# Optimization experiments

Measured on AMD Instinct MI355X. Metric: run time of the kernel, lower is better.

The kernel has to match this reference:

```python
import jax, jax.numpy as jnp
import numpy as np

B, T, C, H = 2, 2048, 1024, 16
HD = C // H  # head dim 64


def setup_inputs() -> dict:
    key = jax.random.key(0)
    k1, k2, k3, k4, k5 = jax.random.split(key, 5)
    s = 0.02
    return {
        "x": jax.random.normal(k1, (B, T, C), dtype=jnp.float32),
        "w_attn": jax.random.normal(k2, (3 * C, C), dtype=jnp.float32) * s,
        "b_attn": jax.random.normal(k3, (3 * C,), dtype=jnp.float32) * s,
        "w_proj": jax.random.normal(k4, (C, C), dtype=jnp.float32) * s,
        "b_proj": jax.random.normal(k5, (C,), dtype=jnp.float32) * s,
    }


def reference(x, w_attn, b_attn, w_proj, b_proj):
    b, t, c = x.shape
    h, hd = H, c // H
    # qkv projection: [B,T,3C]
    qkv = x @ w_attn.T + b_attn
    q, k, v = jnp.split(qkv, 3, axis=-1)
    # [B,H,T,HD]
    q = q.reshape(b, t, h, hd).transpose(0, 2, 1, 3)
    k = k.reshape(b, t, h, hd).transpose(0, 2, 1, 3)
    v = v.reshape(b, t, h, hd).transpose(0, 2, 1, 3)
    scale = 1.0 / jnp.sqrt(jnp.asarray(hd, dtype=x.dtype))
    att = jnp.einsum("bhqd,bhkd->bhqk", q, k) * scale  # [B,H,T,T]
    causal = jnp.tril(jnp.ones((t, t), dtype=bool))
    att = jnp.where(causal, att, jnp.asarray(-jnp.inf, dtype=att.dtype))
    att = jax.nn.softmax(att, axis=-1)
    # dropout p=0.0 (eval): no-op
    y = jnp.einsum("bhqk,bhkd->bhqd", att, v)  # [B,H,T,HD]
    y = y.transpose(0, 2, 1, 3).reshape(b, t, c)
    return y @ w_proj.T + b_proj
```

## Files before the change

kernel.cpp:

```cpp
#include <hip/hip_runtime.h>
#include <hip/hip_bf16.h>

typedef __attribute__((ext_vector_type(4))) float f32x4;
typedef __attribute__((ext_vector_type(8))) short bh8;

#define DEVI static __device__ __forceinline__

constexpr int Bn = 2, T = 2048, C = 1024, H = 16, HD = 64;
constexpr int BH = Bn * H;
constexpr int M  = Bn * T;
constexpr float QSC = 0.125f * 1.44269504088896f;

DEVI unsigned short f2bf(float f) {
  unsigned int u = __builtin_bit_cast(unsigned int, f);
  u += 0x7FFFu + ((u >> 16) & 1u);
  return (unsigned short)(u >> 16);
}

DEVI unsigned int cvtpk(float lo, float hi) {
  unsigned int r;
  asm("v_cvt_pk_bf16_f32 %0, %1, %2" : "=v"(r) : "v"(lo), "v"(hi));
  return r;
}

DEVI void gload16(const void* g, void* l) {
  __builtin_amdgcn_global_load_lds((const __attribute__((address_space(1))) void*)g,
                                   (__attribute__((address_space(3))) void*)l,
                                   16, 0, 0);
}

__global__ __launch_bounds__(256) void cvt_bf16(const float* __restrict__ in,
                                                unsigned short* __restrict__ out,
                                                int n) {
  int i = (blockIdx.x * 256 + threadIdx.x) * 4;
  if (i < n) {
    const float4 v = *(const float4*)(in + i);
    ushort4 o;
    o.x = f2bf(v.x); o.y = f2bf(v.y); o.z = f2bf(v.z); o.w = f2bf(v.w);
    *(ushort4*)(out + i) = o;
  }
}

template <int EPI>
__global__ __launch_bounds__(256) void gemm_bt(
    const unsigned short* __restrict__ A, const unsigned short* __restrict__ Bw,
    const float* __restrict__ bias, int N, int K,
    unsigned short* __restrict__ Qb, unsigned short* __restrict__ Kb,
    unsigned short* __restrict__ Vb, float* __restrict__ Outf) {
  __shared__ unsigned short As[128 * 64];
  __shared__ unsigned short Bs[128 * 64];

  const int tid  = threadIdx.x;
  const int lane = tid & 63;
  const int wid  = tid >> 6;
  const int wm = wid >> 1, wn = wid & 1;
  const int m0 = blockIdx.y * 128;
  const int n0 = blockIdx.x * 128;

  const int srow = lane >> 3;
  const int gp   = lane & 7;

  const unsigned short* Ab = A + (size_t)m0 * K;
  const unsigned short* Bb = Bw + (size_t)n0 * K;

  f32x4 acc[4][4] = {};

  for (int kt = 0; kt < K; kt += 64) {
    __syncthreads();
#pragma unroll
    for (int j = 0; j < 4; ++j) {
      const int row = wid * 32 + j * 8 + srow;
      const int gs  = gp ^ (row & 7);
      gload16(Ab + (size_t)row * K + kt + gs * 8, &As[(wid * 32 + j * 8) * 64]);
    }
#pragma unroll
    for (int j = 0; j < 4; ++j) {
      const int row = wid * 32 + j * 8 + srow;
      const int gs  = gp ^ (row & 7);
      gload16(Bb + (size_t)row * K + kt + gs * 8, &Bs[(wid * 32 + j * 8) * 64]);
    }
    __syncthreads();

#pragma unroll
    for (int kk = 0; kk < 2; ++kk) {
      bh8 af[4], bfr[4];
#pragma unroll
      for (int i = 0; i < 4; ++i) {
        const int row  = wm * 64 + i * 16 + (lane & 15);
        const int gran = kk * 4 + (lane >> 4);
        af[i] = *(const bh8*)&As[row * 64 + ((gran ^ (row & 7)) * 8)];
      }
#pragma unroll
      for (int j = 0; j < 4; ++j) {
        const int row  = wn * 64 + j * 16 + (lane & 15);
        const int gran = kk * 4 + (lane >> 4);
        bfr[j] = *(const bh8*)&Bs[row * 64 + ((gran ^ (row & 7)) * 8)];
      }
#pragma unroll
      for (int i = 0; i < 4; ++i)
#pragma unroll
        for (int j = 0; j < 4; ++j)
          acc[i][j] = __builtin_amdgcn_mfma_f32_16x16x32_bf16(af[i], bfr[j],
                                                              acc[i][j], 0, 0, 0);
    }
  }

  const int rbase = m0 + wm * 64 + ((lane >> 4) << 2);
  const int cbase = n0 + wn * 64 + (lane & 15);

  if (EPI == 0) {
#pragma unroll
    for (int j = 0; j < 4; ++j) {
      const int n = cbase + j * 16;
      const float bv = bias[n];
#pragma unroll
      for (int i = 0; i < 4; ++i)
#pragma unroll
        for (int r = 0; r < 4; ++r) {
          const int m = rbase + i * 16 + r;
          Outf[(size_t)m * N + n] = acc[i][j][r] + bv;
        }
    }
  } else {
#pragma unroll
    for (int j = 0; j < 4; ++j) {
      const int n = cbase + j * 16;
      const float bv = bias[n];
      const int part = n >> 10;
      const int nn = n & 1023;
      const int h = nn >> 6, d = nn & 63;
#pragma unroll
      for (int i = 0; i < 4; ++i)
#pragma unroll
        for (int r = 0; r < 4; ++r) {
          const int m = rbase + i * 16 + r;
          const int b = m >> 11, t = m & (T - 1);
          const int bh = b * H + h;
          const float val = acc[i][j][r] + bv;
          if (part == 0)
            Qb[((size_t)(bh * T + t)) * HD + d] = f2bf(val * QSC);
          else if (part == 1)
            Kb[((size_t)(bh * T + t)) * HD + d] = f2bf(val);
          else {
            const int kp  = t & 127;
            const int kap = (kp & ~31) | (((kp >> 2) & 3) << 3) |
                            (((kp >> 4) & 1) << 2) | (kp & 3);
            const int tp  = (t & ~127) | kap;
            Vb[((size_t)(bh * HD + d)) * T + tp] = f2bf(val);
          }
        }
    }
  }
}

__global__ __launch_bounds__(512, 2) void attn(
    const unsigned short* __restrict__ Qb, const unsigned short* __restrict__ Kb,
    const unsigned short* __restrict__ Vb, unsigned short* __restrict__ Yb) {
  __shared__ unsigned short Ks[2][128 * 64];
  __shared__ unsigned short Vs[2][64 * 128];

  const int tid  = threadIdx.x;
  const int lane = tid & 63;
  const int wid  = tid >> 6;
  const int bh   = blockIdx.y;
  const int b = bh >> 4, h = bh & 15;
  const int qa = blockIdx.x;
  const int na = qa + 1;

  const int l4  = lane >> 4;
  const int l15 = lane & 15;

  const unsigned short* Kbh = Kb + (size_t)bh * T * HD;
  const unsigned short* Vbh = Vb + (size_t)bh * HD * T;

  const int krow0 = wid * 16;
  const int kr    = lane >> 3;
  const int kgp   = lane & 7;
  const int vrow0 = wid * 8;
  const int vr    = lane >> 4;
  const int vgp   = lane & 15;

  bh8 qk0, qk1;
  {
    const size_t qo = ((size_t)(bh * T + qa * 128 + wid * 16 + l15)) * HD + l4 * 8;
    qk0 = *(const bh8*)&Qb[qo];
    qk1 = *(const bh8*)&Qb[qo + 32];
  }

  f32x4 o[4] = {};
  float mcur = -1e30f, lsum = 0.f;

#pragma unroll
  for (int sl = 0; sl < 2; ++sl) {
    const int row = krow0 + sl * 8 + kr;
    gload16(Kbh + (size_t)row * HD + ((kgp ^ (row & 7)) * 8), &Ks[0][(krow0 + sl * 8) * 64]);
  }
#pragma unroll
  for (int sl = 0; sl < 2; ++sl) {
    const int row = vrow0 + sl * 4 + vr;
    gload16(Vbh + (size_t)row * T + ((vgp ^ (row & 15)) * 8), &Vs[0][(vrow0 + sl * 4) * 128]);
  }
  __syncthreads();

  int cur = 0;
  for (int it = 0; it < 17; ++it) {
    if (it < 16) {
      const int nit = it + 1;
      const int nkt = (nit < na ? nit : nit - na) * 128;
#pragma unroll
      for (int sl = 0; sl < 2; ++sl) {
        const int row = krow0 + sl * 8 + kr;
        gload16(Kbh + (size_t)(nkt + row) * HD + ((kgp ^ (row & 7)) * 8),
                &Ks[cur ^ 1][(krow0 + sl * 8) * 64]);
      }
#pragma unroll
      for (int sl = 0; sl < 2; ++sl) {
        const int row = vrow0 + sl * 4 + vr;
        gload16(Vbh + (size_t)row * T + nkt + ((vgp ^ (row & 15)) * 8),
                &Vs[cur ^ 1][(vrow0 + sl * 4) * 128]);
      }
    }

    if (it == na) {
      const float inv = 1.f / lsum;
      const int t = qa * 128 + wid * 16 + l15;
#pragma unroll
      for (int dj = 0; dj < 4; ++dj) {
        ushort4 hw;
        hw.x = f2bf(o[dj][0] * inv); hw.y = f2bf(o[dj][1] * inv);
        hw.z = f2bf(o[dj][2] * inv); hw.w = f2bf(o[dj][3] * inv);
        *(ushort4*)&Yb[((size_t)(b * T + t)) * C + h * HD + dj * 16 + l4 * 4] = hw;
      }
      mcur = -1e30f; lsum = 0.f;
#pragma unroll
      for (int dj = 0; dj < 4; ++dj) o[dj] = f32x4{0.f, 0.f, 0.f, 0.f};
      const size_t qo = ((size_t)(bh * T + (15 - qa) * 128 + wid * 16 + l15)) * HD + l4 * 8;
      qk0 = *(const bh8*)&Qb[qo];
      qk1 = *(const bh8*)&Qb[qo + 32];
    }

    const int qt   = (it < na) ? qa : 15 - qa;
    const int kt   = (it < na ? it : it - na) * 128;
    const bool diag = (kt == qt * 128);

    f32x4 s[8] = {};
#pragma unroll
    for (int kk = 0; kk < 2; ++kk) {
      bh8 kfr[8];
#pragma unroll
      for (int j = 0; j < 8; ++j) {
        const int row  = j * 16 + l15;
        const int gran = kk * 4 + l4;
        kfr[j] = *(const bh8*)&Ks[cur][row * 64 + ((gran ^ (row & 7)) * 8)];
      }
      const bh8 qf = kk ? qk1 : qk0;
      __builtin_amdgcn_s_setprio(1);
#pragma unroll
      for (int j = 0; j < 8; ++j)
        s[j] = __builtin_amdgcn_mfma_f32_16x16x32_bf16(kfr[j], qf, s[j], 0, 0, 0);
      __builtin_amdgcn_s_setprio(0);
    }

    if (diag) {
      const int qoff = wid * 16 + l15;
#pragma unroll
      for (int j = 0; j < 8; ++j)
#pragma unroll
        for (int r = 0; r < 4; ++r) {
          const int kvoff = j * 16 + l4 * 4 + r;
          if (kvoff > qoff) s[j][r] = -1e30f;
        }
    }

    float mx = fmaxf(fmaxf(s[0][0], s[0][1]), fmaxf(s[0][2], s[0][3]));
#pragma unroll
    for (int j = 1; j < 8; ++j)
      mx = fmaxf(mx, fmaxf(fmaxf(s[j][0], s[j][1]), fmaxf(s[j][2], s[j][3])));
    mx = fmaxf(mx, __shfl_xor(mx, 16));
    mx = fmaxf(mx, __shfl_xor(mx, 32));
    if (__any(mx > mcur + 8.f)) {
      const float mnew  = fmaxf(mcur, mx);
      const float alpha = exp2f(mcur - mnew);
      mcur = mnew; lsum *= alpha;
#pragma unroll
      for (int dj = 0; dj < 4; ++dj) o[dj] *= alpha;
    }
    float ps = 0.f;
#pragma unroll
    for (int j = 0; j < 8; ++j)
#pragma unroll
      for (int r = 0; r < 4; ++r) {
        const float p = exp2f(s[j][r] - mcur);
        s[j][r] = p;
        ps += p;
      }
    ps += __shfl_xor(ps, 16);
    ps += __shfl_xor(ps, 32);
    lsum += ps;

#pragma unroll
    for (int kk2 = 0; kk2 < 4; ++kk2) {
      const int gran = kk2 * 4 + l4;
      bh8 vf[4];
#pragma unroll
      for (int dj = 0; dj < 4; ++dj) {
        const int row = dj * 16 + l15;
        vf[dj] = *(const bh8*)&Vs[cur][row * 128 + ((gran ^ (row & 15)) * 8)];
      }
      int4 pw;
      pw.x = cvtpk(s[2 * kk2][0], s[2 * kk2][1]);
      pw.y = cvtpk(s[2 * kk2][2], s[2 * kk2][3]);
      pw.z = cvtpk(s[2 * kk2 + 1][0], s[2 * kk2 + 1][1]);
      pw.w = cvtpk(s[2 * kk2 + 1][2], s[2 * kk2 + 1][3]);
      const bh8 pf = __builtin_bit_cast(bh8, pw);
      __builtin_amdgcn_s_setprio(1);
#pragma unroll
      for (int dj = 0; dj < 4; ++dj)
        o[dj] = __builtin_amdgcn_mfma_f32_16x16x32_bf16(vf[dj], pf, o[dj], 0, 0, 0);
      __builtin_amdgcn_s_setprio(0);
    }

    __syncthreads();
    cur ^= 1;
  }

  {
    const float inv = 1.f / lsum;
    const int t = (15 - qa) * 128 + wid * 16 + l15;
#pragma unroll
    for (int dj = 0; dj < 4; ++dj) {
      ushort4 hw;
      hw.x = f2bf(o[dj][0] * inv); hw.y = f2bf(o[dj][1] * inv);
      hw.z = f2bf(o[dj][2] * inv); hw.w = f2bf(o[dj][3] * inv);
      *(ushort4*)&Yb[((size_t)(b * T + t)) * C + h * HD + dj * 16 + l4 * 4] = hw;
    }
  }
}

extern "C" void kernel_launch(void* const* d_in, const int* in_sizes, int n_in,
                              void* d_out, int out_size, void* d_ws, size_t ws_size,
                              hipStream_t stream) {
  const float* x      = (const float*)d_in[0];
  const float* w_attn = (const float*)d_in[1];
  const float* b_attn = (const float*)d_in[2];
  const float* w_proj = (const float*)d_in[3];
  const float* b_proj = (const float*)d_in[4];
  float* out = (float*)d_out;

  unsigned short* xb  = (unsigned short*)d_ws;
  unsigned short* wab = xb  + (size_t)M * C;
  unsigned short* wpb = wab + (size_t)3 * C * C;
  unsigned short* Qb  = wpb + (size_t)C * C;
  unsigned short* Kb  = Qb  + (size_t)M * C;
  unsigned short* Vb  = Kb  + (size_t)M * C;
  unsigned short* Yb  = xb;

  cvt_bf16<<<dim3((M * C) / 1024), 256, 0, stream>>>(x, xb, M * C);
  cvt_bf16<<<dim3((3 * C * C) / 1024), 256, 0, stream>>>(w_attn, wab, 3 * C * C);
  cvt_bf16<<<dim3((C * C) / 1024), 256, 0, stream>>>(w_proj, wpb, C * C);

  gemm_bt<1><<<dim3(3 * C / 128, M / 128), 256, 0, stream>>>(
      xb, wab, b_attn, 3 * C, C, Qb, Kb, Vb, nullptr);

  attn<<<dim3(8, BH), 512, 0, stream>>>(Qb, Kb, Vb, Yb);

  gemm_bt<0><<<dim3(C / 128, M / 128), 256, 0, stream>>>(
      Yb, wpb, b_proj, C, C, nullptr, nullptr, nullptr, out);
}
```

Baseline: 126.0 us.

## Double-buffer GEMM LDS tiles, fuse conversion kernels, reorder attention grid

The GEMM now double-buffers its LDS tiles. Each iteration issues the global-to-LDS loads for the next K tile before the MFMAs on the current one, and it raises wave priority around the MFMA block. The three fp32-to-bf16 conversion launches are merged into a single kernel that picks its source by index, which saves launch overhead. The attention grid swaps its axes so that blocks for different heads at the same query tile are adjacent, which changes scheduling order and may balance the causal workload better. In exchange, GEMM LDS use doubles, which could lower occupancy.

Measured after the change: 131.6 us. 1.04x slower.

```diff
diff --git a/kernel.cpp b/kernel.cpp
--- a/kernel.cpp
+++ b/kernel.cpp
@@ -29,16 +29,22 @@
                                    16, 0, 0);
 }
 
-__global__ __launch_bounds__(256) void cvt_bf16(const float* __restrict__ in,
-                                                unsigned short* __restrict__ out,
-                                                int n) {
-  int i = (blockIdx.x * 256 + threadIdx.x) * 4;
-  if (i < n) {
-    const float4 v = *(const float4*)(in + i);
-    ushort4 o;
-    o.x = f2bf(v.x); o.y = f2bf(v.y); o.z = f2bf(v.z); o.w = f2bf(v.w);
-    *(ushort4*)(out + i) = o;
-  }
+__global__ __launch_bounds__(256) void cvt_all(const float* __restrict__ x,
+                                               const float* __restrict__ wa,
+                                               const float* __restrict__ wp,
+                                               unsigned short* __restrict__ out) {
+  constexpr size_t n0 = (size_t)M * C;
+  constexpr size_t n1 = n0 + (size_t)3 * C * C;
+  const size_t i = ((size_t)blockIdx.x * 256 + threadIdx.x) * 4;
+  const float* src;
+  size_t off;
+  if (i < n0)      { src = x;  off = i; }
+  else if (i < n1) { src = wa; off = i - n0; }
+  else             { src = wp; off = i - n1; }
+  const float4 v = *(const float4*)(src + off);
+  ushort4 o;
+  o.x = f2bf(v.x); o.y = f2bf(v.y); o.z = f2bf(v.z); o.w = f2bf(v.w);
+  *(ushort4*)(out + i) = o;
 }
 
 template <int EPI>
@@ -47,8 +53,8 @@
     const float* __restrict__ bias, int N, int K,
     unsigned short* __restrict__ Qb, unsigned short* __restrict__ Kb,
     unsigned short* __restrict__ Vb, float* __restrict__ Outf) {
-  __shared__ unsigned short As[128 * 64];
-  __shared__ unsigned short Bs[128 * 64];
+  __shared__ unsigned short As[2][128 * 64];
+  __shared__ unsigned short Bs[2][128 * 64];
 
   const int tid  = threadIdx.x;
   const int lane = tid & 63;
@@ -65,21 +71,28 @@
 
   f32x4 acc[4][4] = {};
 
+#pragma unroll
+  for (int j = 0; j < 4; ++j) {
+    const int row = wid * 32 + j * 8 + srow;
+    const int gs  = gp ^ (row & 7);
+    gload16(Ab + (size_t)row * K + gs * 8, &As[0][(wid * 32 + j * 8) * 64]);
+    gload16(Bb + (size_t)row * K + gs * 8, &Bs[0][(wid * 32 + j * 8) * 64]);
+  }
+  __syncthreads();
+
+  int cur = 0;
   for (int kt = 0; kt < K; kt += 64) {
-    __syncthreads();
-#pragma unroll
-    for (int j = 0; j < 4; ++j) {
-      const int row = wid * 32 + j * 8 + srow;
-      const int gs  = gp ^ (row & 7);
-      gload16(Ab + (size_t)row * K + kt + gs * 8, &As[(wid * 32 + j * 8) * 64]);
-    }
-#pragma unroll
-    for (int j = 0; j < 4; ++j) {
-      const int row = wid * 32 + j * 8 + srow;
-      const int gs  = gp ^ (row & 7);
-      gload16(Bb + (size_t)row * K + kt + gs * 8, &Bs[(wid * 32 + j * 8) * 64]);
-    }
-    __syncthreads();
+    if (kt + 64 < K) {
+#pragma unroll
+      for (int j = 0; j < 4; ++j) {
+        const int row = wid * 32 + j * 8 + srow;
+        const int gs  = gp ^ (row & 7);
+        gload16(Ab + (size_t)row * K + kt + 64 + gs * 8,
+                &As[cur ^ 1][(wid * 32 + j * 8) * 64]);
+        gload16(Bb + (size_t)row * K + kt + 64 + gs * 8,
+                &Bs[cur ^ 1][(wid * 32 + j * 8) * 64]);
+      }
+    }
 
 #pragma unroll
     for (int kk = 0; kk < 2; ++kk) {
@@ -88,21 +101,26 @@
       for (int i = 0; i < 4; ++i) {
         const int row  = wm * 64 + i * 16 + (lane & 15);
         const int gran = kk * 4 + (lane >> 4);
-        af[i] = *(const bh8*)&As[row * 64 + ((gran ^ (row & 7)) * 8)];
+        af[i] = *(const bh8*)&As[cur][row * 64 + ((gran ^ (row & 7)) * 8)];
       }
 #pragma unroll
       for (int j = 0; j < 4; ++j) {
         const int row  = wn * 64 + j * 16 + (lane & 15);
         const int gran = kk * 4 + (lane >> 4);
-        bfr[j] = *(const bh8*)&Bs[row * 64 + ((gran ^ (row & 7)) * 8)];
-      }
+        bfr[j] = *(const bh8*)&Bs[cur][row * 64 + ((gran ^ (row & 7)) * 8)];
+      }
+      __builtin_amdgcn_s_setprio(1);
 #pragma unroll
       for (int i = 0; i < 4; ++i)
 #pragma unroll
         for (int j = 0; j < 4; ++j)
           acc[i][j] = __builtin_amdgcn_mfma_f32_16x16x32_bf16(af[i], bfr[j],
                                                               acc[i][j], 0, 0, 0);
-    }
+      __builtin_amdgcn_s_setprio(0);
+    }
+
+    __syncthreads();
+    cur ^= 1;
   }
 
   const int rbase = m0 + wm * 64 + ((lane >> 4) << 2);
@@ -162,9 +180,9 @@
   const int tid  = threadIdx.x;
   const int lane = tid & 63;
   const int wid  = tid >> 6;
-  const int bh   = blockIdx.y;
+  const int bh   = blockIdx.x;
   const int b = bh >> 4, h = bh & 15;
-  const int qa = blockIdx.x;
+  const int qa = blockIdx.y;
   const int na = qa + 1;
 
   const int l4  = lane >> 4;
@@ -355,14 +373,13 @@
   unsigned short* Vb  = Kb  + (size_t)M * C;
   unsigned short* Yb  = xb;
 
-  cvt_bf16<<<dim3((M * C) / 1024), 256, 0, stream>>>(x, xb, M * C);
-  cvt_bf16<<<dim3((3 * C * C) / 1024), 256, 0, stream>>>(w_attn, wab, 3 * C * C);
-  cvt_bf16<<<dim3((C * C) / 1024), 256, 0, stream>>>(w_proj, wpb, C * C);
+  constexpr int CVT_BLOCKS = (M * C + 3 * C * C + C * C) / 1024;
+  cvt_all<<<dim3(CVT_BLOCKS), 256, 0, stream>>>(x, w_attn, w_proj, xb);
 
   gemm_bt<1><<<dim3(3 * C / 128, M / 128), 256, 0, stream>>>(
       xb, wab, b_attn, 3 * C, C, Qb, Kb, Vb, nullptr);
 
-  attn<<<dim3(8, BH), 512, 0, stream>>>(Qb, Kb, Vb, Yb);
+  attn<<<dim3(BH, 8), 512, 0, stream>>>(Qb, Kb, Vb, Yb);
 
   gemm_bt<0><<<dim3(C / 128, M / 128), 256, 0, stream>>>(
       Yb, wpb, b_proj, C, C, nullptr, nullptr, nullptr, out);
```
